# Performance work log

Hardware: AMD Instinct MI355X
Metric: run time of the kernel (lower is better)

Reference implementation:

```python
import jax, jax.numpy as jnp
import numpy as np

EPS = 1e-06

def rmsnorm(x, w):
    x32 = x.astype(jnp.float32)
    var = jnp.mean(x32 * x32, axis=-1, keepdims=True)
    return w * (x32 * jax.lax.rsqrt(var + EPS)).astype(x.dtype)

def setup_inputs() -> dict:
    B, T, C = 16, 256, 16
    token_dim, text_dim = 1024, 512
    key = jax.random.key(0)
    ks = jax.random.split(key, 8)
    token_embeds = jax.random.normal(ks[0], (B, T, token_dim), dtype=jnp.float32)
    char_embeds = jax.random.normal(ks[1], (B, T, C, text_dim), dtype=jnp.float32)
    filler_embed = jax.random.normal(ks[2], (text_dim,), dtype=jnp.float32)
    mask = jax.random.randint(ks[3], (B, T, C), 0, 2).astype(bool)
    mask = mask.at[0].set(True)  # force max valid count == T*C (static output shape)
    token_ids_mask = jnp.ones((B, T), dtype=bool)
    # xavier-uniform-ish weights
    def xav(k, fan_out, fan_in, gain=1.0):
        lim = gain * np.sqrt(6.0 / (fan_in + fan_out))
        return jax.random.uniform(k, (fan_out, fan_in), jnp.float32, -lim, lim)
    W_down = xav(ks[4], text_dim, token_dim)
    W_proj = xav(ks[5], 3, text_dim, gain=0.2)
    W_fusion = xav(ks[6], text_dim, text_dim)
    w_pre = jnp.ones((token_dim,), jnp.float32)
    w_tok = jnp.ones((text_dim,), jnp.float32)
    w_char = jnp.ones((text_dim,), jnp.float32)
    return {"token_embeds": token_embeds, "token_ids_mask": token_ids_mask,
            "char_embeds": char_embeds, "char_ids_mask": mask,
            "filler_embed": filler_embed, "w_pre": w_pre, "w_tok": w_tok,
            "w_char": w_char, "W_down": W_down, "W_proj": W_proj,
            "W_fusion": W_fusion, "max_valid_chars": T * C}

def reference(token_embeds, token_ids_mask, char_embeds, char_ids_mask,
              filler_embed, w_pre, w_tok, w_char, W_down, W_proj, W_fusion,
              max_valid_chars):
    B, T, C, d = char_embeds.shape
    MV = int(max_valid_chars)
    tok = rmsnorm(token_embeds, w_pre)                       # [B,T,token_dim]
    feats = rmsnorm(jnp.einsum('btk,dk->btd', tok, W_down), w_tok)  # [B,T,d]
    params = jnp.einsum('btd,pd->btp', jax.nn.silu(feats), W_proj)  # [B,T,3]
    scale = params[..., 0][:, :, None, None]                 # [B,T,1,1]
    shift = params[..., 1][:, :, None, None]
    gate = jax.nn.sigmoid(params[..., 2][:, :, None, None])
    cn = rmsnorm(char_embeds, w_char)                        # [B,T,C,d]
    fused = jnp.einsum('btcd,ed->btce', jax.nn.silu(cn * (1.0 + scale) + shift), W_fusion)
    fused = gate * fused + (1.0 - gate) * cn                 # [B,T,C,d]
    flat = fused.reshape(B, T * C, d)
    m = char_ids_mask.reshape(B, T * C).astype(jnp.int32)
    pos = jnp.cumsum(m, axis=1) - 1                          # dest within row
    offs = jnp.arange(B, dtype=jnp.int32)[:, None] * MV
    idx = jnp.where(m > 0, offs + pos, B * MV)               # invalid -> dump slot
    buf = jnp.broadcast_to(filler_embed, (B * MV + 1, d))
    buf = buf.at[idx.reshape(-1)].set(flat.reshape(-1, d))
    return buf[: B * MV].reshape(B, MV, d)
```

## Files before the change

kernel.cpp:

```cpp
#include <hip/hip_runtime.h>
#include <cstdint>
#include <cstddef>

#define EPS 1e-6f

typedef short bf16x8 __attribute__((ext_vector_type(8)));
typedef float f32x4  __attribute__((ext_vector_type(4)));

__device__ __forceinline__ short f2bf(float x) {
    uint32_t u = __builtin_bit_cast(uint32_t, x);
    return (short)((u + 0x7FFFu + ((u >> 16) & 1u)) >> 16);
}

__global__ __launch_bounds__(256) void k_scan(const void* __restrict__ maskp,
                                              int* __restrict__ v_list,
                                              int* __restrict__ counts) {
    __shared__ int sc[256];
    __shared__ int mode_s;
    const int tid = threadIdx.x;
    const int b = blockIdx.x;
    const uint32_t* mi = (const uint32_t*)maskp;
    const uint8_t* mb = (const uint8_t*)maskp;

    if (tid == 0) mode_s = 0;
    __syncthreads();
    int bad = 0;
    for (int k = tid; k < 1024; k += 256) bad |= (mi[k] > 1u) ? 1 : 0;
    if (bad) mode_s = 1;
    __syncthreads();
    const int byte_mode = mode_s;

    int base = 0;
    for (int chunk = 0; chunk < 16; ++chunk) {
        const int i = chunk * 256 + tid;
        int m;
        if (byte_mode) m = mb[(b << 12) + i] ? 1 : 0;
        else           m = mi[(b << 12) + i] ? 1 : 0;
        sc[tid] = m;
        __syncthreads();
        for (int off = 1; off < 256; off <<= 1) {
            int v = sc[tid];
            int a = (tid >= off) ? sc[tid - off] : 0;
            __syncthreads();
            sc[tid] = v + a;
            __syncthreads();
        }
        const int incl = sc[tid];
        const int tot = sc[255];
        if (m) v_list[(b << 12) + base + incl - 1] = i;
        base += tot;
        __syncthreads();
    }
    if (tid == 0) counts[b] = base;
}

__global__ __launch_bounds__(256) void k_conv(const float* __restrict__ src,
                                              short* __restrict__ dst, int n4) {
    const int gid = blockIdx.x * 256 + threadIdx.x;
    if (gid >= n4) return;
    const float4 v = ((const float4*)src)[gid];
    short4 o;
    o.x = f2bf(v.x); o.y = f2bf(v.y); o.z = f2bf(v.z); o.w = f2bf(v.w);
    ((short4*)dst)[gid] = o;
}

__global__ __launch_bounds__(256) void k_tokprep(const float* __restrict__ tokens,
                                                 const float* __restrict__ w_pre,
                                                 short* __restrict__ tokbf) {
    const int tid = threadIdx.x, lane = tid & 63, wave = tid >> 6;
    const int row = blockIdx.x * 4 + wave;
    const float* xp = tokens + (size_t)row * 1024 + lane * 16;
    float4 x[4];
#pragma unroll
    for (int q = 0; q < 4; ++q) x[q] = *(const float4*)&xp[q * 4];
    float ss = 0.f;
#pragma unroll
    for (int q = 0; q < 4; ++q)
        ss += x[q].x * x[q].x + x[q].y * x[q].y + x[q].z * x[q].z + x[q].w * x[q].w;
#pragma unroll
    for (int off = 32; off > 0; off >>= 1) ss += __shfl_down(ss, off);
    ss = __shfl(ss, 0);
    const float r = rsqrtf(ss * (1.0f / 1024.0f) + EPS);
    const float* wp = w_pre + lane * 16;
    short* op = tokbf + (size_t)row * 1024 + lane * 16;
#pragma unroll
    for (int h = 0; h < 2; ++h) {
        bf16x8 o;
#pragma unroll
        for (int q = 0; q < 2; ++q) {
            const float4 wv = *(const float4*)&wp[h * 8 + q * 4];
            const float4 xv = x[h * 2 + q];
            o[q * 4 + 0] = f2bf(xv.x * wv.x * r);
            o[q * 4 + 1] = f2bf(xv.y * wv.y * r);
            o[q * 4 + 2] = f2bf(xv.z * wv.z * r);
            o[q * 4 + 3] = f2bf(xv.w * wv.w * r);
        }
        *(bf16x8*)&op[h * 8] = o;
    }
}

__global__ __launch_bounds__(256) void k_gemm_tok(const short* __restrict__ tokbf,
                                                  const short* __restrict__ Wdbf,
                                                  float* __restrict__ feats) {
    __shared__ short As[128 * 32];
    __shared__ short Bs[128 * 32];
    const int tid = threadIdx.x, lane = tid & 63, w = tid >> 6;
    const int mt = blockIdx.x >> 2, nt = blockIdx.x & 3;
    const int wm = w >> 1, wn = w & 1;
    const short* hA = tokbf + (size_t)mt * 128 * 1024;
    const short* wB = Wdbf + (size_t)nt * 128 * 1024;

    f32x4 acc[4][4];
#pragma unroll
    for (int mi = 0; mi < 4; ++mi)
#pragma unroll
        for (int ni = 0; ni < 4; ++ni) acc[mi][ni] = (f32x4)0.f;

    const int rA = lane & 15, q8 = (lane >> 4) * 8;
    for (int kk = 0; kk < 1024; kk += 32) {
#pragma unroll
        for (int q = 0; q < 2; ++q) {
            const int cid = (w * 2 + q) * 64 + lane;
            const int r = cid >> 2, kc = cid & 3;
            const size_t go = (size_t)r * 1024 + kk + kc * 8;
            __builtin_amdgcn_global_load_lds(
                (const __attribute__((address_space(1))) uint32_t*)(hA + go),
                (__attribute__((address_space(3))) uint32_t*)&As[(w * 2 + q) * 512], 16, 0, 0);
            __builtin_amdgcn_global_load_lds(
                (const __attribute__((address_space(1))) uint32_t*)(wB + go),
                (__attribute__((address_space(3))) uint32_t*)&Bs[(w * 2 + q) * 512], 16, 0, 0);
        }
        __syncthreads();
        bf16x8 af[4], bfr[4];
#pragma unroll
        for (int mi = 0; mi < 4; ++mi)
            af[mi] = *(const bf16x8*)&As[(wm * 64 + mi * 16 + rA) * 32 + q8];
#pragma unroll
        for (int ni = 0; ni < 4; ++ni)
            bfr[ni] = *(const bf16x8*)&Bs[(wn * 64 + ni * 16 + rA) * 32 + q8];
#pragma unroll
        for (int mi = 0; mi < 4; ++mi)
#pragma unroll
            for (int ni = 0; ni < 4; ++ni)
                acc[mi][ni] = __builtin_amdgcn_mfma_f32_16x16x32_bf16(af[mi], bfr[ni], acc[mi][ni], 0, 0, 0);
        __syncthreads();
    }
    const int rowb = mt * 128 + wm * 64 + (lane >> 4) * 4;
    const int colb = nt * 128 + wn * 64 + (lane & 15);
#pragma unroll
    for (int mi = 0; mi < 4; ++mi)
#pragma unroll
        for (int ni = 0; ni < 4; ++ni)
#pragma unroll
            for (int rg = 0; rg < 4; ++rg)
                feats[(size_t)(rowb + mi * 16 + rg) * 512 + colb + ni * 16] = acc[mi][ni][rg];
}

__global__ __launch_bounds__(64) void k_params(
    const float* __restrict__ feats_pre, const float* __restrict__ w_tok,
    const float* __restrict__ W_proj, float* __restrict__ params) {
    const int tk = blockIdx.x;
    const int lane = threadIdx.x;
    const int d0 = lane * 8;
    const float* fp = feats_pre + (size_t)tk * 512 + d0;
    const float4 f0 = *(const float4*)&fp[0];
    const float4 f1 = *(const float4*)&fp[4];
    float ss = f0.x * f0.x + f0.y * f0.y + f0.z * f0.z + f0.w * f0.w
             + f1.x * f1.x + f1.y * f1.y + f1.z * f1.z + f1.w * f1.w;
#pragma unroll
    for (int off = 32; off > 0; off >>= 1) ss += __shfl_down(ss, off);
    ss = __shfl(ss, 0);
    const float rms = rsqrtf(ss * (1.0f / 512.0f) + EPS);

    const float4 wt0 = *(const float4*)&w_tok[d0];
    const float4 wt1 = *(const float4*)&w_tok[d0 + 4];
    float fv[8] = {f0.x, f0.y, f0.z, f0.w, f1.x, f1.y, f1.z, f1.w};
    float wv[8] = {wt0.x, wt0.y, wt0.z, wt0.w, wt1.x, wt1.y, wt1.z, wt1.w};
    float s[8];
#pragma unroll
    for (int j = 0; j < 8; ++j) {
        const float v = fv[j] * wv[j] * rms;
        s[j] = v / (1.0f + expf(-v));
    }
    float p[3];
#pragma unroll
    for (int q = 0; q < 3; ++q) {
        const float* Wp = W_proj + (size_t)q * 512 + d0;
        const float4 a = *(const float4*)&Wp[0];
        const float4 c = *(const float4*)&Wp[4];
        p[q] = s[0] * a.x + s[1] * a.y + s[2] * a.z + s[3] * a.w
             + s[4] * c.x + s[5] * c.y + s[6] * c.z + s[7] * c.w;
#pragma unroll
        for (int off = 32; off > 0; off >>= 1) p[q] += __shfl_down(p[q], off);
    }
    if (lane == 0) {
        float* po = params + (size_t)tk * 4;
        po[0] = 1.0f + p[0];
        po[1] = p[1];
        po[2] = 1.0f / (1.0f + expf(-p[2]));
    }
}

__global__ __launch_bounds__(256) void k_prep(
    const float* __restrict__ chars, const float* __restrict__ w_char,
    const float* __restrict__ params, const int* __restrict__ v_list,
    const int* __restrict__ counts, short* __restrict__ hb,
    float* __restrict__ rms_l, float* __restrict__ g_l) {
    const int tid = threadIdx.x, lane = tid & 63, wave = tid >> 6;
    const int b = blockIdx.x >> 10;
    const int j = (blockIdx.x & 1023) * 4 + wave;
    const int cnt = counts[b];
    const int cpad = (cnt + 127) & ~127;
    if (j >= cpad) return;
    short* hrow = hb + ((size_t)(b << 12) + j) * 512 + lane * 8;
    if (j >= cnt) {
        *(bf16x8*)hrow = (bf16x8)0;
        return;
    }
    const int i = v_list[(b << 12) + j];
    const float* xp = chars + ((size_t)(b << 12) + i) * 512 + lane * 8;
    const float4 x0 = *(const float4*)&xp[0];
    const float4 x1 = *(const float4*)&xp[4];
    float ss = x0.x * x0.x + x0.y * x0.y + x0.z * x0.z + x0.w * x0.w
             + x1.x * x1.x + x1.y * x1.y + x1.z * x1.z + x1.w * x1.w;
#pragma unroll
    for (int off = 32; off > 0; off >>= 1) ss += __shfl_down(ss, off);
    ss = __shfl(ss, 0);
    const float rms = rsqrtf(ss * (1.0f / 512.0f) + EPS);
    const float* pp = params + (size_t)((b << 8) + (i >> 4)) * 4;
    const float s1 = pp[0], sh = pp[1], g = pp[2];
    const float4 w0 = *(const float4*)&w_char[lane * 8];
    const float4 w1 = *(const float4*)&w_char[lane * 8 + 4];
    float xv[8] = {x0.x, x0.y, x0.z, x0.w, x1.x, x1.y, x1.z, x1.w};
    float wv[8] = {w0.x, w0.y, w0.z, w0.w, w1.x, w1.y, w1.z, w1.w};
    bf16x8 o;
#pragma unroll
    for (int q = 0; q < 8; ++q) {
        const float cn = wv[q] * xv[q] * rms;
        const float a = cn * s1 + sh;
        o[q] = f2bf(a / (1.0f + expf(-a)));
    }
    *(bf16x8*)hrow = o;
    if (lane == 0) {
        rms_l[(b << 12) + j] = rms;
        g_l[(b << 12) + j] = g;
    }
}

__global__ __launch_bounds__(256) void k_fill(
    const float* __restrict__ filler, const int* __restrict__ counts,
    float* __restrict__ out) {
    const int gid = blockIdx.x * 256 + threadIdx.x;
    const size_t e4 = (size_t)gid * 4;
    const int slot = gid >> 7;
    const int b = slot >> 12;
    const int j = slot & 4095;
    if (j >= counts[b]) {
        const int e0 = (int)(e4 & 511);
        *(float4*)&out[e4] = *(const float4*)&filler[e0];
    }
}

__global__ __launch_bounds__(256) void k_gemm_fus(
    const short* __restrict__ hb, const short* __restrict__ Wbf,
    const float* __restrict__ chars, const float* __restrict__ w_char,
    const float* __restrict__ rms_l, const float* __restrict__ g_l,
    const int* __restrict__ v_list, const int* __restrict__ counts,
    float* __restrict__ out) {
    __shared__ short As[128 * 32];
    __shared__ short Bs[128 * 32];
    __shared__ float g_s[128], rms_s[128];
    __shared__ int idx_s[128];
    const int tid = threadIdx.x, lane = tid & 63, w = tid >> 6;
    const int b = blockIdx.x >> 7;
    const int mt = (blockIdx.x >> 2) & 31;
    const int nt = blockIdx.x & 3;
    const int cnt = counts[b];
    const int row0 = mt * 128;
    if (row0 >= cnt) return;
    const int wm = w >> 1, wn = w & 1;

    if (tid < 128) {
        const int j = row0 + tid;
        const bool valid = j < cnt;
        idx_s[tid] = valid ? v_list[(b << 12) + j] : 0;
        g_s[tid]   = valid ? g_l[(b << 12) + j] : 0.f;
        rms_s[tid] = valid ? rms_l[(b << 12) + j] : 0.f;
    }

    const short* hA = hb + ((size_t)(b << 12) + row0) * 512;
    const short* wB = Wbf + (size_t)nt * 128 * 512;

    f32x4 acc[4][4];
#pragma unroll
    for (int mi = 0; mi < 4; ++mi)
#pragma unroll
        for (int ni = 0; ni < 4; ++ni) acc[mi][ni] = (f32x4)0.f;

    const int rA = lane & 15, q8 = (lane >> 4) * 8;
    for (int kk = 0; kk < 512; kk += 32) {
#pragma unroll
        for (int q = 0; q < 2; ++q) {
            const int cid = (w * 2 + q) * 64 + lane;
            const int r = cid >> 2, kc = cid & 3;
            const size_t go = (size_t)r * 512 + kk + kc * 8;
            __builtin_amdgcn_global_load_lds(
                (const __attribute__((address_space(1))) uint32_t*)(hA + go),
                (__attribute__((address_space(3))) uint32_t*)&As[(w * 2 + q) * 512], 16, 0, 0);
            __builtin_amdgcn_global_load_lds(
                (const __attribute__((address_space(1))) uint32_t*)(wB + go),
                (__attribute__((address_space(3))) uint32_t*)&Bs[(w * 2 + q) * 512], 16, 0, 0);
        }
        __syncthreads();
        bf16x8 af[4], bfr[4];
#pragma unroll
        for (int mi = 0; mi < 4; ++mi)
            af[mi] = *(const bf16x8*)&As[(wm * 64 + mi * 16 + rA) * 32 + q8];
#pragma unroll
        for (int ni = 0; ni < 4; ++ni)
            bfr[ni] = *(const bf16x8*)&Bs[(wn * 64 + ni * 16 + rA) * 32 + q8];
#pragma unroll
        for (int mi = 0; mi < 4; ++mi)
#pragma unroll
            for (int ni = 0; ni < 4; ++ni)
                acc[mi][ni] = __builtin_amdgcn_mfma_f32_16x16x32_bf16(af[mi], bfr[ni], acc[mi][ni], 0, 0, 0);
        __syncthreads();
    }

    const int colb = nt * 128 + wn * 64 + (lane & 15);
    float wcv[4];
#pragma unroll
    for (int ni = 0; ni < 4; ++ni) wcv[ni] = w_char[colb + ni * 16];
#pragma unroll
    for (int mi = 0; mi < 4; ++mi) {
#pragma unroll
        for (int rg = 0; rg < 4; ++rg) {
            const int jl = wm * 64 + mi * 16 + (lane >> 4) * 4 + rg;
            const int j = row0 + jl;
            if (j < cnt) {
                const float g = g_s[jl], rm = rms_s[jl];
                const size_t xrow = ((size_t)(b << 12) + idx_s[jl]) * 512;
                const size_t orow = ((size_t)(b << 12) + j) * 512;
#pragma unroll
                for (int ni = 0; ni < 4; ++ni) {
                    const int col = colb + ni * 16;
                    const float x = chars[xrow + col];
                    const float cn = wcv[ni] * x * rm;
                    out[orow + col] = g * acc[mi][ni][rg] + (1.0f - g) * cn;
                }
            }
        }
    }
}

extern "C" void kernel_launch(void* const* d_in, const int* in_sizes, int n_in,
                              void* d_out, int out_size, void* d_ws, size_t ws_size,
                              hipStream_t stream) {
    const float* tokens = (const float*)d_in[0];
    const float* chars  = (const float*)d_in[2];
    const void*  cmask  = d_in[3];
    const float* filler = (const float*)d_in[4];
    const float* w_pre  = (const float*)d_in[5];
    const float* w_tok  = (const float*)d_in[6];
    const float* w_char = (const float*)d_in[7];
    const float* W_down = (const float*)d_in[8];
    const float* W_proj = (const float*)d_in[9];
    const float* W_fus  = (const float*)d_in[10];
    float* out = (float*)d_out;

    float* feats_pre = (float*)d_ws;
    float* params    = feats_pre + (size_t)4096 * 512;
    int*   counts    = (int*)(params + (size_t)4096 * 4);
    int*   v_list    = counts + 16;
    float* rms_l     = (float*)(v_list + 65536);
    float* g_l       = rms_l + 65536;
    short* Wbf       = (short*)(g_l + 65536);
    short* hb        = Wbf + (size_t)512 * 512;
    short* tokbf     = hb + (size_t)16 * 4096 * 512;
    short* Wdbf      = tokbf + (size_t)4096 * 1024;

    k_scan<<<16, 256, 0, stream>>>(cmask, v_list, counts);
    k_conv<<<256, 256, 0, stream>>>(W_fus, Wbf, 65536);
    k_conv<<<512, 256, 0, stream>>>(W_down, Wdbf, 131072);
    k_tokprep<<<1024, 256, 0, stream>>>(tokens, w_pre, tokbf);
    k_gemm_tok<<<128, 256, 0, stream>>>(tokbf, Wdbf, feats_pre);
    k_params<<<4096, 64, 0, stream>>>(feats_pre, w_tok, W_proj, params);
    k_prep<<<16384, 256, 0, stream>>>(chars, w_char, params, v_list, counts, hb, rms_l, g_l);
    k_fill<<<32768, 256, 0, stream>>>(filler, counts, out);
    k_gemm_fus<<<2048, 256, 0, stream>>>(hb, Wbf, chars, w_char, rms_l, g_l, v_list, counts, out);
}
```

Baseline: 368.6 us.

## Fuse filler writes into fusion GEMM, split-K token GEMM, faster scan

Drops the separate k_fill kernel. The fusion GEMM now writes filler rows itself: whole tiles for blocks past the valid count, and single rows inside partial tiles. This avoids writing the whole output twice. The token GEMM is split into two K halves to double the grid to 256 blocks, and k_params sums the two partial results. The mask scan is rewritten as a single-pass wave-shuffle scan over 1024 threads, and the two weight conversions are merged into one launch. The cost is extra workspace for the split-K partials and extra reads in k_params.

```diff
diff --git a/kernel.cpp b/kernel.cpp
--- a/kernel.cpp
+++ b/kernel.cpp
@@ -12,56 +12,80 @@
     return (short)((u + 0x7FFFu + ((u >> 16) & 1u)) >> 16);
 }
 
-__global__ __launch_bounds__(256) void k_scan(const void* __restrict__ maskp,
-                                              int* __restrict__ v_list,
-                                              int* __restrict__ counts) {
-    __shared__ int sc[256];
+__global__ __launch_bounds__(1024) void k_scan(const void* __restrict__ maskp,
+                                               int* __restrict__ v_list,
+                                               int* __restrict__ counts) {
+    __shared__ int wtot[16];
+    __shared__ int woff[16];
     __shared__ int mode_s;
-    const int tid = threadIdx.x;
+    const int tid = threadIdx.x, lane = tid & 63, wave = tid >> 6;
     const int b = blockIdx.x;
-    const uint32_t* mi = (const uint32_t*)maskp;
-    const uint8_t* mb = (const uint8_t*)maskp;
 
     if (tid == 0) mode_s = 0;
     __syncthreads();
-    int bad = 0;
-    for (int k = tid; k < 1024; k += 256) bad |= (mi[k] > 1u) ? 1 : 0;
-    if (bad) mode_s = 1;
+    {
+        const int bad = (((const uint32_t*)maskp)[tid & 1023] > 1u) ? 1 : 0;
+        if (bad) mode_s = 1;
+    }
     __syncthreads();
     const int byte_mode = mode_s;
 
-    int base = 0;
-    for (int chunk = 0; chunk < 16; ++chunk) {
-        const int i = chunk * 256 + tid;
-        int m;
-        if (byte_mode) m = mb[(b << 12) + i] ? 1 : 0;
-        else           m = mi[(b << 12) + i] ? 1 : 0;
-        sc[tid] = m;
-        __syncthreads();
-        for (int off = 1; off < 256; off <<= 1) {
-            int v = sc[tid];
-            int a = (tid >= off) ? sc[tid - off] : 0;
-            __syncthreads();
-            sc[tid] = v + a;
-            __syncthreads();
-        }
-        const int incl = sc[tid];
-        const int tot = sc[255];
-        if (m) v_list[(b << 12) + base + incl - 1] = i;
-        base += tot;
-        __syncthreads();
-    }
-    if (tid == 0) counts[b] = base;
-}
-
-__global__ __launch_bounds__(256) void k_conv(const float* __restrict__ src,
-                                              short* __restrict__ dst, int n4) {
+    int f0, f1, f2, f3;
+    if (byte_mode) {
+        const uint32_t v = ((const uint32_t*)maskp)[(b << 10) + tid];
+        f0 = (v & 0x000000ffu) != 0;
+        f1 = (v & 0x0000ff00u) != 0;
+        f2 = (v & 0x00ff0000u) != 0;
+        f3 = (v & 0xff000000u) != 0;
+    } else {
+        const uint4 v = ((const uint4*)maskp)[(b << 10) + tid];
+        f0 = v.x != 0; f1 = v.y != 0; f2 = v.z != 0; f3 = v.w != 0;
+    }
+    const int c = f0 + f1 + f2 + f3;
+
+    int incl = c;
+#pragma unroll
+    for (int off = 1; off < 64; off <<= 1) {
+        const int n = __shfl_up(incl, off);
+        if (lane >= off) incl += n;
+    }
+    if (lane == 63) wtot[wave] = incl;
+    __syncthreads();
+    if (tid == 0) {
+        int run = 0;
+#pragma unroll
+        for (int wv = 0; wv < 16; ++wv) { woff[wv] = run; run += wtot[wv]; }
+        counts[b] = run;
+    }
+    __syncthreads();
+
+    int base = woff[wave] + incl - c;
+    const int i0 = tid * 4;
+    int* vl = v_list + (b << 12);
+    if (f0) vl[base++] = i0;
+    if (f1) vl[base++] = i0 + 1;
+    if (f2) vl[base++] = i0 + 2;
+    if (f3) vl[base++] = i0 + 3;
+}
+
+__global__ __launch_bounds__(256) void k_conv2(const float* __restrict__ srcA,
+                                               short* __restrict__ dstA, int n4a,
+                                               const float* __restrict__ srcB,
+                                               short* __restrict__ dstB, int n4b) {
     const int gid = blockIdx.x * 256 + threadIdx.x;
-    if (gid >= n4) return;
-    const float4 v = ((const float4*)src)[gid];
+    const float* s;
+    short* d;
+    int i;
+    if (gid < n4a) { s = srcA; d = dstA; i = gid; }
+    else {
+        i = gid - n4a;
+        if (i >= n4b) return;
+        s = srcB; d = dstB;
+    }
+    const float4 v = ((const float4*)s)[i];
     short4 o;
     o.x = f2bf(v.x); o.y = f2bf(v.y); o.z = f2bf(v.z); o.w = f2bf(v.w);
-    ((short4*)dst)[gid] = o;
+    ((short4*)d)[i] = o;
 }
 
 __global__ __launch_bounds__(256) void k_tokprep(const float* __restrict__ tokens,
@@ -105,8 +129,10 @@
     __shared__ short As[128 * 32];
     __shared__ short Bs[128 * 32];
     const int tid = threadIdx.x, lane = tid & 63, w = tid >> 6;
-    const int mt = blockIdx.x >> 2, nt = blockIdx.x & 3;
+    const int kt = blockIdx.x >> 7;
+    const int mt = (blockIdx.x >> 2) & 31, nt = blockIdx.x & 3;
     const int wm = w >> 1, wn = w & 1;
+    const int kbase = kt * 512;
     const short* hA = tokbf + (size_t)mt * 128 * 1024;
     const short* wB = Wdbf + (size_t)nt * 128 * 1024;
 
@@ -117,12 +143,12 @@
         for (int ni = 0; ni < 4; ++ni) acc[mi][ni] = (f32x4)0.f;
 
     const int rA = lane & 15, q8 = (lane >> 4) * 8;
-    for (int kk = 0; kk < 1024; kk += 32) {
+    for (int kk = 0; kk < 512; kk += 32) {
 #pragma unroll
         for (int q = 0; q < 2; ++q) {
             const int cid = (w * 2 + q) * 64 + lane;
             const int r = cid >> 2, kc = cid & 3;
-            const size_t go = (size_t)r * 1024 + kk + kc * 8;
+            const size_t go = (size_t)r * 1024 + kbase + kk + kc * 8;
             __builtin_amdgcn_global_load_lds(
                 (const __attribute__((address_space(1))) uint32_t*)(hA + go),
                 (__attribute__((address_space(3))) uint32_t*)&As[(w * 2 + q) * 512], 16, 0, 0);
@@ -145,6 +171,7 @@
                 acc[mi][ni] = __builtin_amdgcn_mfma_f32_16x16x32_bf16(af[mi], bfr[ni], acc[mi][ni], 0, 0, 0);
         __syncthreads();
     }
+    float* fo = feats + (size_t)kt * 4096 * 512;
     const int rowb = mt * 128 + wm * 64 + (lane >> 4) * 4;
     const int colb = nt * 128 + wn * 64 + (lane & 15);
 #pragma unroll
@@ -153,7 +180,7 @@
         for (int ni = 0; ni < 4; ++ni)
 #pragma unroll
             for (int rg = 0; rg < 4; ++rg)
-                feats[(size_t)(rowb + mi * 16 + rg) * 512 + colb + ni * 16] = acc[mi][ni][rg];
+                fo[(size_t)(rowb + mi * 16 + rg) * 512 + colb + ni * 16] = acc[mi][ni][rg];
 }
 
 __global__ __launch_bounds__(64) void k_params(
@@ -162,9 +189,14 @@
     const int tk = blockIdx.x;
     const int lane = threadIdx.x;
     const int d0 = lane * 8;
-    const float* fp = feats_pre + (size_t)tk * 512 + d0;
-    const float4 f0 = *(const float4*)&fp[0];
-    const float4 f1 = *(const float4*)&fp[4];
+    const float* fp0 = feats_pre + (size_t)tk * 512 + d0;
+    const float* fp1 = fp0 + (size_t)4096 * 512;
+    const float4 a0 = *(const float4*)&fp0[0];
+    const float4 a1 = *(const float4*)&fp0[4];
+    const float4 b0 = *(const float4*)&fp1[0];
+    const float4 b1 = *(const float4*)&fp1[4];
+    const float4 f0 = make_float4(a0.x + b0.x, a0.y + b0.y, a0.z + b0.z, a0.w + b0.w);
+    const float4 f1 = make_float4(a1.x + b1.x, a1.y + b1.y, a1.z + b1.z, a1.w + b1.w);
     float ss = f0.x * f0.x + f0.y * f0.y + f0.z * f0.z + f0.w * f0.w
              + f1.x * f1.x + f1.y * f1.y + f1.z * f1.z + f1.w * f1.w;
 #pragma unroll
@@ -247,26 +279,12 @@
     }
 }
 
-__global__ __launch_bounds__(256) void k_fill(
-    const float* __restrict__ filler, const int* __restrict__ counts,
-    float* __restrict__ out) {
-    const int gid = blockIdx.x * 256 + threadIdx.x;
-    const size_t e4 = (size_t)gid * 4;
-    const int slot = gid >> 7;
-    const int b = slot >> 12;
-    const int j = slot & 4095;
-    if (j >= counts[b]) {
-        const int e0 = (int)(e4 & 511);
-        *(float4*)&out[e4] = *(const float4*)&filler[e0];
-    }
-}
-
 __global__ __launch_bounds__(256) void k_gemm_fus(
     const short* __restrict__ hb, const short* __restrict__ Wbf,
     const float* __restrict__ chars, const float* __restrict__ w_char,
     const float* __restrict__ rms_l, const float* __restrict__ g_l,
     const int* __restrict__ v_list, const int* __restrict__ counts,
-    float* __restrict__ out) {
+    const float* __restrict__ filler, float* __restrict__ out) {
     __shared__ short As[128 * 32];
     __shared__ short Bs[128 * 32];
     __shared__ float g_s[128], rms_s[128];
@@ -277,7 +295,15 @@
     const int nt = blockIdx.x & 3;
     const int cnt = counts[b];
     const int row0 = mt * 128;
-    if (row0 >= cnt) return;
+    if (row0 >= cnt) {
+        const int colb = nt * 128;
+        const float4 f = ((const float4*)(filler + colb))[tid & 31];
+        float* o0 = out + ((size_t)(b << 12) + row0) * 512 + colb + (tid & 31) * 4;
+#pragma unroll
+        for (int r = (tid >> 5); r < 128; r += 8)
+            *(float4*)&o0[(size_t)r * 512] = f;
+        return;
+    }
     const int wm = w >> 1, wn = w & 1;
 
     if (tid < 128) {
@@ -337,16 +363,22 @@
         for (int rg = 0; rg < 4; ++rg) {
             const int jl = wm * 64 + mi * 16 + (lane >> 4) * 4 + rg;
             const int j = row0 + jl;
+            const size_t orow = ((size_t)(b << 12) + j) * 512;
             if (j < cnt) {
                 const float g = g_s[jl], rm = rms_s[jl];
                 const size_t xrow = ((size_t)(b << 12) + idx_s[jl]) * 512;
-                const size_t orow = ((size_t)(b << 12) + j) * 512;
 #pragma unroll
                 for (int ni = 0; ni < 4; ++ni) {
                     const int col = colb + ni * 16;
                     const float x = chars[xrow + col];
                     const float cn = wcv[ni] * x * rm;
                     out[orow + col] = g * acc[mi][ni][rg] + (1.0f - g) * cn;
+                }
+            } else {
+#pragma unroll
+                for (int ni = 0; ni < 4; ++ni) {
+                    const int col = colb + ni * 16;
+                    out[orow + col] = filler[col];
                 }
             }
         }
@@ -369,7 +401,7 @@
     float* out = (float*)d_out;
 
     float* feats_pre = (float*)d_ws;
-    float* params    = feats_pre + (size_t)4096 * 512;
+    float* params    = feats_pre + (size_t)2 * 4096 * 512;
     int*   counts    = (int*)(params + (size_t)4096 * 4);
     int*   v_list    = counts + 16;
     float* rms_l     = (float*)(v_list + 65536);
@@ -379,13 +411,11 @@
     short* tokbf     = hb + (size_t)16 * 4096 * 512;
     short* Wdbf      = tokbf + (size_t)4096 * 1024;
 
-    k_scan<<<16, 256, 0, stream>>>(cmask, v_list, counts);
-    k_conv<<<256, 256, 0, stream>>>(W_fus, Wbf, 65536);
-    k_conv<<<512, 256, 0, stream>>>(W_down, Wdbf, 131072);
+    k_scan<<<16, 1024, 0, stream>>>(cmask, v_list, counts);
+    k_conv2<<<768, 256, 0, stream>>>(W_fus, Wbf, 65536, W_down, Wdbf, 131072);
     k_tokprep<<<1024, 256, 0, stream>>>(tokens, w_pre, tokbf);
-    k_gemm_tok<<<128, 256, 0, stream>>>(tokbf, Wdbf, feats_pre);
+    k_gemm_tok<<<256, 256, 0, stream>>>(tokbf, Wdbf, feats_pre);
     k_params<<<4096, 64, 0, stream>>>(feats_pre, w_tok, W_proj, params);
     k_prep<<<16384, 256, 0, stream>>>(chars, w_char, params, v_list, counts, hb, rms_l, g_l);
-    k_fill<<<32768, 256, 0, stream>>>(filler, counts, out);
-    k_gemm_fus<<<2048, 256, 0, stream>>>(hb, Wbf, chars, w_char, rms_l, g_l, v_list, counts, out);
-}
+    k_gemm_fus<<<2048, 256, 0, stream>>>(hb, Wbf, chars, w_char, rms_l, g_l, v_list, counts, filler, out);
+}
```

New measurement: 339.8 us. -7.8%, faster.
